# Kernel optimization log

Measured on AMD Instinct MI355X. Metric: run time of the kernel, lower is better.

The kernel has to match this reference:

```python
import jax, jax.numpy as jnp
import numpy as np

N = 300000   # number of occupied voxels (sparse tensor rows)
L = 100      # grid side length -> 1e6 cells, occupancy 0.3
C = 32       # channels (channelwise/depthwise conv)
KS = 3       # kernel_size per axis
D = 3        # spatial dimension
R = (KS - 1) // 2


def _build_sparse_structure():
    """Sample N unique voxel coords and build kernel maps (edge lists) like
    MinkowskiEngine's coordinate manager: for each kernel offset, pairs
    (in_idx, out_idx) such that coords[in_idx] == coords[out_idx] + offset."""
    rng = np.random.default_rng(0)
    flat = rng.choice(L ** 3, size=N, replace=False)
    coords = np.stack([flat // (L * L), (flat // L) % L, flat % L], axis=1).astype(np.int32)
    keys = flat.astype(np.int64)
    order = np.argsort(keys)
    sk = keys[order]
    out_ids = np.arange(N, dtype=np.int64)
    in_list, out_list = [], []
    for dx in range(-R, R + 1):
        for dy in range(-R, R + 1):
            for dz in range(-R, R + 1):
                nx = coords[:, 0].astype(np.int64) + dx
                ny = coords[:, 1].astype(np.int64) + dy
                nz = coords[:, 2].astype(np.int64) + dz
                inb = (nx >= 0) & (nx < L) & (ny >= 0) & (ny < L) & (nz >= 0) & (nz < L)
                nk = (nx * L + ny) * L + nz
                pos = np.searchsorted(sk, nk)
                pos_c = np.clip(pos, 0, N - 1)
                ok = inb & (sk[pos_c] == nk)
                in_list.append(order[pos_c[ok]])
                out_list.append(out_ids[ok])
    in_idx = np.concatenate(in_list).astype(np.int32)
    out_idx = np.concatenate(out_list).astype(np.int32)
    return coords, in_idx, out_idx


def setup_inputs() -> dict:
    coords, in_idx, out_idx = _build_sparse_structure()
    key = jax.random.key(0)
    k1, k2 = jax.random.split(key)
    in_feats = jax.random.normal(k1, (N, C), dtype=jnp.float32)
    kernel = jax.random.normal(k2, (KS ** D, C), dtype=jnp.float32)  # depthwise kernel
    return {
        "coords": jnp.asarray(coords),
        "in_idx": jnp.asarray(in_idx),
        "out_idx": jnp.asarray(out_idx),
        "in_feats": in_feats,
        "kernel": kernel,
    }


def reference(coords, in_idx, out_idx, in_feats, kernel):
    # index_array = KS ** flip(arange(D)) -> [9, 3, 1] for KS=3, D=3
    index_pow = jnp.array([KS ** (D - 1 - i) for i in range(D)], dtype=jnp.int32)
    # tensor_stride = 1; kernel_coord = (C_in - C_out)//1 + (KS-1)//2, per edge [E, D]
    kernel_coord = coords[in_idx] - coords[out_idx] + R
    k1d = jnp.sum(index_pow[None, :] * kernel_coord, axis=1)  # [E] in [0, KS**D)
    # gather-multiply-scatter: out_F[out] += in_feats[in] * kernel[k1d]
    out_F = jnp.zeros_like(in_feats).at[out_idx].add(in_feats[in_idx] * kernel[k1d])
    return out_F
```

## Files before the change

kernel.cpp:

```cpp
#include <hip/hip_runtime.h>

#define NCH 32
#define GROUPS 8
#define KVOL 27
#define LG 100
#define LP 102
#define RGN 5
#define NRGN 20
#define NREGIONS (NRGN * NRGN * NRGN)
#define BSIDE 7
#define BVOL 343
#define CELLS 125
#define LSTR 29

__global__ void build_dense(const int* __restrict__ coords,
                            int* __restrict__ dense, int N) {
    int i = blockIdx.x * blockDim.x + threadIdx.x;
    if (i >= N) return;
    int x = coords[3 * i + 0];
    int y = coords[3 * i + 1];
    int z = coords[3 * i + 2];
    dense[((size_t)(x + 1) * LP + (y + 1)) * LP + (z + 1)] = i + 1;
}

__global__ __launch_bounds__(256) void gather_conv_region(
        const int* __restrict__ dense,
        const float4* __restrict__ in_feats4,
        const float4* __restrict__ kernel4,
        float4* __restrict__ out4) {
    __shared__ float4 kw[(KVOL + 1) * GROUPS];
    __shared__ int brick[BVOL];
    __shared__ int rows[CELLS];
    __shared__ int cnts[CELLS];
    __shared__ int list[CELLS * LSTR];
    __shared__ int cnt;

    int tid = threadIdx.x;

    int b = blockIdx.x;
    const int per = NREGIONS >> 3;
    int r = (b & 7) * per + (b >> 3);

    if (tid == 0) cnt = 0;
    for (int i = tid; i < (KVOL + 1) * GROUPS; i += 256)
        kw[i] = (i < KVOL * GROUPS) ? kernel4[i]
                                    : make_float4(0.f, 0.f, 0.f, 0.f);

    int bx = r / (NRGN * NRGN);
    int by = (r / NRGN) % NRGN;
    int bz = r % NRGN;
    int ox = bx * RGN, oy = by * RGN, oz = bz * RGN;

    for (int i = tid; i < BVOL; i += 256) {
        int lx = i / (BSIDE * BSIDE), ly = (i / BSIDE) % BSIDE, lz = i % BSIDE;
        brick[i] = dense[((size_t)(ox + lx) * LP + (oy + ly)) * LP + (oz + lz)];
    }
    __syncthreads();

    if (tid < CELLS) {
        int cx = tid / (RGN * RGN), cy = (tid / RGN) % RGN, cz = tid % RGN;
        int bidx = (cx + 1) * (BSIDE * BSIDE) + (cy + 1) * BSIDE + (cz + 1);
        int v = brick[bidx];
        if (v > 0) {
            int p = atomicAdd(&cnt, 1);
            int myrow = v - 1;
            rows[p] = myrow;
            int j = 0;
            #pragma unroll
            for (int k = 0; k < KVOL; ++k) {
                int dx = k / 9 - 1, dy = (k / 3) % 3 - 1, dz = k % 3 - 1;
                int nb = brick[bidx + dx * (BSIDE * BSIDE) + dy * BSIDE + dz];
                if (nb > 0) list[p * LSTR + (j++)] = ((nb - 1) << 5) | k;
            }
            while (j & 3) list[p * LSTR + (j++)] = (myrow << 5) | KVOL;
            cnts[p] = j;
        }
    }
    __syncthreads();

    int n  = cnt;
    int lr = tid >> 3;
    int g  = tid & 7;
    for (int base = 0; base < n; base += 32) {
        int lo = base + lr;
        if (lo < n) {
            int cr = cnts[lo];
            const int* tl = &list[lo * LSTR];
            float4 acc = make_float4(0.f, 0.f, 0.f, 0.f);
            for (int j = 0; j < cr; j += 4) {
                int e0 = tl[j + 0], e1 = tl[j + 1];
                int e2 = tl[j + 2], e3 = tl[j + 3];
                float4 f0 = in_feats4[(size_t)(e0 >> 5) * GROUPS + g];
                float4 f1 = in_feats4[(size_t)(e1 >> 5) * GROUPS + g];
                float4 f2 = in_feats4[(size_t)(e2 >> 5) * GROUPS + g];
                float4 f3 = in_feats4[(size_t)(e3 >> 5) * GROUPS + g];
                float4 w0 = kw[(e0 & 31) * GROUPS + g];
                float4 w1 = kw[(e1 & 31) * GROUPS + g];
                float4 w2 = kw[(e2 & 31) * GROUPS + g];
                float4 w3 = kw[(e3 & 31) * GROUPS + g];
                acc.x += f0.x * w0.x; acc.y += f0.y * w0.y;
                acc.z += f0.z * w0.z; acc.w += f0.w * w0.w;
                acc.x += f1.x * w1.x; acc.y += f1.y * w1.y;
                acc.z += f1.z * w1.z; acc.w += f1.w * w1.w;
                acc.x += f2.x * w2.x; acc.y += f2.y * w2.y;
                acc.z += f2.z * w2.z; acc.w += f2.w * w2.w;
                acc.x += f3.x * w3.x; acc.y += f3.y * w3.y;
                acc.z += f3.z * w3.z; acc.w += f3.w * w3.w;
            }
            out4[(size_t)rows[lo] * GROUPS + g] = acc;
        }
    }
}

__global__ void mink_conv_scatter(const int* __restrict__ coords,
                                  const int* __restrict__ in_idx,
                                  const int* __restrict__ out_idx,
                                  const float4* __restrict__ in_feats4,
                                  const float4* __restrict__ kernel4,
                                  float* __restrict__ out,
                                  int E) {
    __shared__ float4 kw[KVOL * GROUPS];
    for (int i = threadIdx.x; i < KVOL * GROUPS; i += blockDim.x)
        kw[i] = kernel4[i];
    __syncthreads();
    int t = blockIdx.x * blockDim.x + threadIdx.x;
    if (t >= E * GROUPS) return;
    int e = t >> 3, g = t & 7;
    int vi = in_idx[e], vo = out_idx[e];
    int c0 = coords[vi * 3 + 0] - coords[vo * 3 + 0] + 1;
    int c1 = coords[vi * 3 + 1] - coords[vo * 3 + 1] + 1;
    int c2 = coords[vi * 3 + 2] - coords[vo * 3 + 2] + 1;
    int k1d = (c0 * 3 + c1) * 3 + c2;
    float4 f = in_feats4[vi * GROUPS + g];
    float4 w = kw[k1d * GROUPS + g];
    float* o = out + vo * NCH + g * 4;
    atomicAdd(o + 0, f.x * w.x);
    atomicAdd(o + 1, f.y * w.y);
    atomicAdd(o + 2, f.z * w.z);
    atomicAdd(o + 3, f.w * w.w);
}

extern "C" void kernel_launch(void* const* d_in, const int* in_sizes, int n_in,
                              void* d_out, int out_size, void* d_ws, size_t ws_size,
                              hipStream_t stream) {
    const int*   coords   = (const int*)d_in[0];
    const int*   in_idx   = (const int*)d_in[1];
    const int*   out_idx  = (const int*)d_in[2];
    const float* in_feats = (const float*)d_in[3];
    const float* kernel   = (const float*)d_in[4];

    const int E     = in_sizes[1];
    const int Nrows = out_size / NCH;

    const size_t dense_bytes = (size_t)LP * LP * LP * sizeof(int);

    if (ws_size >= dense_bytes) {
        int* dense = (int*)d_ws;
        hipMemsetAsync(dense, 0, dense_bytes, stream);

        int block = 256;
        int grid1 = (Nrows + block - 1) / block;
        build_dense<<<grid1, block, 0, stream>>>(coords, dense, Nrows);

        gather_conv_region<<<NREGIONS, 256, 0, stream>>>(
            dense, (const float4*)in_feats, (const float4*)kernel,
            (float4*)d_out);
    } else {
        hipMemsetAsync(d_out, 0, (size_t)out_size * sizeof(float), stream);
        int total = E * GROUPS;
        int block = 256;
        int grid  = (total + block - 1) / block;
        mink_conv_scatter<<<grid, block, 0, stream>>>(
            coords, in_idx, out_idx,
            (const float4*)in_feats, (const float4*)kernel,
            (float*)d_out, E);
    }
}
```

Baseline: 144.2 us.

## Split region gather into compaction pass and load-balanced flat gather kernel

```diff
diff --git a/kernel.cpp b/kernel.cpp
--- a/kernel.cpp
+++ b/kernel.cpp
@@ -11,7 +11,13 @@
 #define BSIDE 7
 #define BVOL 343
 #define CELLS 125
-#define LSTR 29
+#define LSTR 28
+#define DUMMY 27
+#define SLOTS 32
+
+static __device__ __forceinline__ void fma4(float4& a, float4 f, float4 w) {
+    a.x += f.x * w.x; a.y += f.y * w.y; a.z += f.z * w.z; a.w += f.w * w.w;
+}
 
 __global__ void build_dense(const int* __restrict__ coords,
                             int* __restrict__ dense, int N) {
@@ -23,6 +29,111 @@
     dense[((size_t)(x + 1) * LP + (y + 1)) * LP + (z + 1)] = i + 1;
 }
 
+__global__ __launch_bounds__(256) void compact_region(
+        const int* __restrict__ dense,
+        int* __restrict__ gctr,
+        int* __restrict__ rows_g,
+        int* __restrict__ offcnt_g,
+        int* __restrict__ list_g) {
+    __shared__ int brick[BVOL];
+    __shared__ int rows_l[CELLS], offs_l[CELLS], cnts_l[CELLS];
+    __shared__ int lds_list[CELLS * LSTR];
+    __shared__ int cnt, taptot, rowbase, tapbase;
+
+    int tid = threadIdx.x;
+    int r = blockIdx.x;
+    if (tid == 0) { cnt = 0; taptot = 0; }
+
+    int bx = r / (NRGN * NRGN);
+    int by = (r / NRGN) % NRGN;
+    int bz = r % NRGN;
+    int ox = bx * RGN, oy = by * RGN, oz = bz * RGN;
+
+    for (int i = tid; i < BVOL; i += 256) {
+        int lx = i / (BSIDE * BSIDE), ly = (i / BSIDE) % BSIDE, lz = i % BSIDE;
+        brick[i] = dense[((size_t)(ox + lx) * LP + (oy + ly)) * LP + (oz + lz)];
+    }
+    __syncthreads();
+
+    if (tid < CELLS) {
+        int cx = tid / (RGN * RGN), cy = (tid / RGN) % RGN, cz = tid % RGN;
+        int bidx = (cx + 1) * (BSIDE * BSIDE) + (cy + 1) * BSIDE + (cz + 1);
+        int v = brick[bidx];
+        if (v > 0) {
+            int p = atomicAdd(&cnt, 1);
+            rows_l[p] = v - 1;
+            int j = 0;
+            #pragma unroll
+            for (int k = 0; k < KVOL; ++k) {
+                int dx = k / 9 - 1, dy = (k / 3) % 3 - 1, dz = k % 3 - 1;
+                int nb = brick[bidx + dx * (BSIDE * BSIDE) + dy * BSIDE + dz];
+                if (nb > 0) lds_list[p * LSTR + (j++)] = ((nb - 1) << 5) | k;
+            }
+            while (j & 3) lds_list[p * LSTR + (j++)] = DUMMY;
+            cnts_l[p] = j;
+            offs_l[p] = atomicAdd(&taptot, j);
+        }
+    }
+    __syncthreads();
+
+    if (tid == 0) {
+        rowbase = atomicAdd(&gctr[0], cnt);
+        tapbase = atomicAdd(&gctr[1], taptot);
+    }
+    __syncthreads();
+
+    if (tid < cnt) {
+        int off = tapbase + offs_l[tid];
+        int jend = cnts_l[tid];
+        rows_g[rowbase + tid] = rows_l[tid];
+        offcnt_g[rowbase + tid] = (off << 3) | (jend >> 2);
+        for (int j = 0; j < jend; ++j)
+            list_g[off + j] = lds_list[tid * LSTR + j];
+    }
+}
+
+__global__ __launch_bounds__(256) void gather_flat(
+        const int* __restrict__ rows_g,
+        const int* __restrict__ offcnt_g,
+        const int* __restrict__ list_g,
+        const float4* __restrict__ in_feats4,
+        const float4* __restrict__ kernel4,
+        float4* __restrict__ out4,
+        int Nrows) {
+    __shared__ float4 kw[(KVOL + 1) * GROUPS];
+    int tid = threadIdx.x;
+    for (int i = tid; i < (KVOL + 1) * GROUPS; i += 256)
+        kw[i] = (i < KVOL * GROUPS) ? kernel4[i]
+                                    : make_float4(0.f, 0.f, 0.f, 0.f);
+    __syncthreads();
+
+    int sid = blockIdx.x * SLOTS + (tid >> 3);
+    int g   = tid & 7;
+    if (sid >= Nrows) return;
+
+    int row  = rows_g[sid];
+    int oc   = offcnt_g[sid];
+    int nq   = oc & 7;
+    const int4* tl = (const int4*)(list_g + (oc >> 3));
+
+    float4 acc = make_float4(0.f, 0.f, 0.f, 0.f);
+    for (int jq = 0; jq < nq; ++jq) {
+        int4 t = tl[jq];
+        float4 f0 = in_feats4[(size_t)(t.x >> 5) * GROUPS + g];
+        float4 f1 = in_feats4[(size_t)(t.y >> 5) * GROUPS + g];
+        float4 f2 = in_feats4[(size_t)(t.z >> 5) * GROUPS + g];
+        float4 f3 = in_feats4[(size_t)(t.w >> 5) * GROUPS + g];
+        float4 w0 = kw[(t.x & 31) * GROUPS + g];
+        float4 w1 = kw[(t.y & 31) * GROUPS + g];
+        float4 w2 = kw[(t.z & 31) * GROUPS + g];
+        float4 w3 = kw[(t.w & 31) * GROUPS + g];
+        fma4(acc, f0, w0); fma4(acc, f1, w1);
+        fma4(acc, f2, w2); fma4(acc, f3, w3);
+    }
+    out4[(size_t)row * GROUPS + g] = acc;
+}
+
+#define LSTR5 29
 __global__ __launch_bounds__(256) void gather_conv_region(
         const int* __restrict__ dense,
         const float4* __restrict__ in_feats4,
@@ -32,80 +143,60 @@
     __shared__ int brick[BVOL];
     __shared__ int rows[CELLS];
     __shared__ int cnts[CELLS];
-    __shared__ int list[CELLS * LSTR];
+    __shared__ int list[CELLS * LSTR5];
     __shared__ int cnt;
 
     int tid = threadIdx.x;
-
-    int b = blockIdx.x;
-    const int per = NREGIONS >> 3;
-    int r = (b & 7) * per + (b >> 3);
-
+    int r = blockIdx.x;
     if (tid == 0) cnt = 0;
     for (int i = tid; i < (KVOL + 1) * GROUPS; i += 256)
         kw[i] = (i < KVOL * GROUPS) ? kernel4[i]
                                     : make_float4(0.f, 0.f, 0.f, 0.f);
-
     int bx = r / (NRGN * NRGN);
     int by = (r / NRGN) % NRGN;
     int bz = r % NRGN;
     int ox = bx * RGN, oy = by * RGN, oz = bz * RGN;
-
     for (int i = tid; i < BVOL; i += 256) {
         int lx = i / (BSIDE * BSIDE), ly = (i / BSIDE) % BSIDE, lz = i % BSIDE;
         brick[i] = dense[((size_t)(ox + lx) * LP + (oy + ly)) * LP + (oz + lz)];
     }
     __syncthreads();
-
     if (tid < CELLS) {
         int cx = tid / (RGN * RGN), cy = (tid / RGN) % RGN, cz = tid % RGN;
         int bidx = (cx + 1) * (BSIDE * BSIDE) + (cy + 1) * BSIDE + (cz + 1);
         int v = brick[bidx];
         if (v > 0) {
             int p = atomicAdd(&cnt, 1);
-            int myrow = v - 1;
-            rows[p] = myrow;
+            rows[p] = v - 1;
             int j = 0;
             #pragma unroll
             for (int k = 0; k < KVOL; ++k) {
                 int dx = k / 9 - 1, dy = (k / 3) % 3 - 1, dz = k % 3 - 1;
                 int nb = brick[bidx + dx * (BSIDE * BSIDE) + dy * BSIDE + dz];
-                if (nb > 0) list[p * LSTR + (j++)] = ((nb - 1) << 5) | k;
+                if (nb > 0) list[p * LSTR5 + (j++)] = ((nb - 1) << 5) | k;
             }
-            while (j & 3) list[p * LSTR + (j++)] = (myrow << 5) | KVOL;
+            while (j & 3) list[p * LSTR5 + (j++)] = DUMMY;
             cnts[p] = j;
         }
     }
     __syncthreads();
-
-    int n  = cnt;
-    int lr = tid >> 3;
-    int g  = tid & 7;
+    int n = cnt, lr = tid >> 3, g = tid & 7;
     for (int base = 0; base < n; base += 32) {
         int lo = base + lr;
         if (lo < n) {
-            int cr = cnts[lo];
-            const int* tl = &list[lo * LSTR];
+            int jend = cnts[lo];
+            const int* tl = &list[lo * LSTR5];
             float4 acc = make_float4(0.f, 0.f, 0.f, 0.f);
-            for (int j = 0; j < cr; j += 4) {
-                int e0 = tl[j + 0], e1 = tl[j + 1];
-                int e2 = tl[j + 2], e3 = tl[j + 3];
+            for (int j = 0; j < jend; j += 4) {
+                int e0 = tl[j], e1 = tl[j+1], e2 = tl[j+2], e3 = tl[j+3];
                 float4 f0 = in_feats4[(size_t)(e0 >> 5) * GROUPS + g];
                 float4 f1 = in_feats4[(size_t)(e1 >> 5) * GROUPS + g];
                 float4 f2 = in_feats4[(size_t)(e2 >> 5) * GROUPS + g];
                 float4 f3 = in_feats4[(size_t)(e3 >> 5) * GROUPS + g];
-                float4 w0 = kw[(e0 & 31) * GROUPS + g];
-                float4 w1 = kw[(e1 & 31) * GROUPS + g];
-                float4 w2 = kw[(e2 & 31) * GROUPS + g];
-                float4 w3 = kw[(e3 & 31) * GROUPS + g];
-                acc.x += f0.x * w0.x; acc.y += f0.y * w0.y;
-                acc.z += f0.z * w0.z; acc.w += f0.w * w0.w;
-                acc.x += f1.x * w1.x; acc.y += f1.y * w1.y;
-                acc.z += f1.z * w1.z; acc.w += f1.w * w1.w;
-                acc.x += f2.x * w2.x; acc.y += f2.y * w2.y;
-                acc.z += f2.z * w2.z; acc.w += f2.w * w2.w;
-                acc.x += f3.x * w3.x; acc.y += f3.y * w3.y;
-                acc.z += f3.z * w3.z; acc.w += f3.w * w3.w;
+                fma4(acc, f0, kw[(e0 & 31) * GROUPS + g]);
+                fma4(acc, f1, kw[(e1 & 31) * GROUPS + g]);
+                fma4(acc, f2, kw[(e2 & 31) * GROUPS + g]);
+                fma4(acc, f3, kw[(e3 & 31) * GROUPS + g]);
             }
             out4[(size_t)rows[lo] * GROUPS + g] = acc;
         }
@@ -119,9 +210,9 @@
                                   const float4* __restrict__ kernel4,
                                   float* __restrict__ out,
                                   int E) {
-    __shared__ float4 kw[KVOL * GROUPS];
+    __shared__ float4 kwf[KVOL * GROUPS];
     for (int i = threadIdx.x; i < KVOL * GROUPS; i += blockDim.x)
-        kw[i] = kernel4[i];
+        kwf[i] = kernel4[i];
     __syncthreads();
     int t = blockIdx.x * blockDim.x + threadIdx.x;
     if (t >= E * GROUPS) return;
@@ -132,13 +223,15 @@
     int c2 = coords[vi * 3 + 2] - coords[vo * 3 + 2] + 1;
     int k1d = (c0 * 3 + c1) * 3 + c2;
     float4 f = in_feats4[vi * GROUPS + g];
-    float4 w = kw[k1d * GROUPS + g];
+    float4 w = kwf[k1d * GROUPS + g];
     float* o = out + vo * NCH + g * 4;
     atomicAdd(o + 0, f.x * w.x);
     atomicAdd(o + 1, f.y * w.y);
     atomicAdd(o + 2, f.z * w.z);
     atomicAdd(o + 3, f.w * w.w);
 }
+
+static inline size_t align256(size_t x) { return (x + 255) & ~(size_t)255; }
 
 extern "C" void kernel_launch(void* const* d_in, const int* in_sizes, int n_in,
                               void* d_out, int out_size, void* d_ws, size_t ws_size,
@@ -154,14 +247,44 @@
 
     const size_t dense_bytes = (size_t)LP * LP * LP * sizeof(int);
 
-    if (ws_size >= dense_bytes) {
-        int* dense = (int*)d_ws;
+    size_t o_dense  = 0;
+    size_t o_gctr   = align256(o_dense + dense_bytes);
+    size_t o_rows   = align256(o_gctr + 256);
+    size_t o_offcnt = align256(o_rows + (size_t)Nrows * 4);
+    size_t o_list   = align256(o_offcnt + (size_t)Nrows * 4);
+    size_t list_cap = ((size_t)E + 3ull * Nrows + 4096) * 4;
+    size_t need2    = o_list + list_cap;
+
+    char* ws = (char*)d_ws;
+
+    if (ws_size >= need2) {
+        int* dense  = (int*)(ws + o_dense);
+        int* gctr   = (int*)(ws + o_gctr);
+        int* rows_g = (int*)(ws + o_rows);
+        int* offcnt = (int*)(ws + o_offcnt);
+        int* list_g = (int*)(ws + o_list);
+
         hipMemsetAsync(dense, 0, dense_bytes, stream);
+        hipMemsetAsync(gctr, 0, 256, stream);
 
         int block = 256;
         int grid1 = (Nrows + block - 1) / block;
         build_dense<<<grid1, block, 0, stream>>>(coords, dense, Nrows);
 
+        compact_region<<<NREGIONS, 256, 0, stream>>>(
+            dense, gctr, rows_g, offcnt, list_g);
+
+        int grid3 = (Nrows + SLOTS - 1) / SLOTS;
+        gather_flat<<<grid3, 256, 0, stream>>>(
+            rows_g, offcnt, list_g,
+            (const float4*)in_feats, (const float4*)kernel,
+            (float4*)d_out, Nrows);
+    } else if (ws_size >= dense_bytes) {
+        int* dense = (int*)d_ws;
+        hipMemsetAsync(dense, 0, dense_bytes, stream);
+        int block = 256;
+        int grid1 = (Nrows + block - 1) / block;
+        build_dense<<<grid1, block, 0, stream>>>(coords, dense, Nrows);
         gather_conv_region<<<NREGIONS, 256, 0, stream>>>(
             dense, (const float4*)in_feats, (const float4*)kernel,
             (float4*)d_out);
```

Result: slower. 326.7 us (+126.6%).
